# Kernel optimization log

Hardware: AMD Instinct MI355X
Metric: run time of the kernel (lower is better)

## Reference

```python
import jax, jax.numpy as jnp
import numpy as np

B, N, E, H, HEADS = 4, 10000, 160000, 128, 4
NEG_SLOPE = 0.2  # PyG GATConv default
LN_EPS = 1e-5


def setup_inputs() -> dict:
    key = jax.random.key(0)
    ks = jax.random.split(key, 24)
    inp = {}
    inp["node_embeddings"] = jax.random.normal(ks[0], (B, N, H), dtype=jnp.float32)
    inp["src_index"] = jax.random.randint(ks[1], (B, E), 0, N)
    inp["tgt_index"] = jax.random.randint(ks[2], (B, E), 0, N)
    sc = 1.0 / np.sqrt(H)
    for i in range(3):
        j = 3 + 3 * i
        inp[f"W{i+1}"] = jax.random.normal(ks[j], (H, HEADS * H), dtype=jnp.float32) * sc
        inp[f"att_src{i+1}"] = jax.random.normal(ks[j + 1], (HEADS, H), dtype=jnp.float32) * sc
        inp[f"att_dst{i+1}"] = jax.random.normal(ks[j + 2], (HEADS, H), dtype=jnp.float32) * sc
        inp[f"bias{i+1}"] = jnp.zeros((H,), dtype=jnp.float32)
    inp["ln1_g"] = jnp.ones((H,), dtype=jnp.float32)
    inp["ln1_b"] = jnp.zeros((H,), dtype=jnp.float32)
    inp["ln2_g"] = jnp.ones((H,), dtype=jnp.float32)
    inp["ln2_b"] = jnp.zeros((H,), dtype=jnp.float32)
    return inp


def _layer_norm(x, g, b):
    mu = jnp.mean(x, axis=-1, keepdims=True)
    var = jnp.mean((x - mu) ** 2, axis=-1, keepdims=True)
    return (x - mu) * jax.lax.rsqrt(var + LN_EPS) * g + b


def _gat(x, src, tgt, W, a_s, a_d, b):
    # x: [N, H]; src/tgt: [E'] (self-loops already appended). eval mode -> no dropout.
    h = (x @ W).reshape(N, HEADS, H)               # [N, heads, H]
    e_src = jnp.einsum('nhc,hc->nh', h, a_s)       # [N, heads]
    e_dst = jnp.einsum('nhc,hc->nh', h, a_d)
    e = jax.nn.leaky_relu(e_src[src] + e_dst[tgt], NEG_SLOPE)  # [E', heads]
    m = jax.ops.segment_max(e, tgt, num_segments=N)            # per-target max
    ex = jnp.exp(e - m[tgt])
    s = jax.ops.segment_sum(ex, tgt, num_segments=N)
    alpha = ex / s[tgt]                                        # [E', heads]
    out = jax.ops.segment_sum(alpha[:, :, None] * h[src], tgt, num_segments=N)
    return out.mean(axis=1) + b                                # concat=False -> head mean


def reference(node_embeddings, src_index, tgt_index,
              W1, att_src1, att_dst1, bias1,
              W2, att_src2, att_dst2, bias2,
              W3, att_src3, att_dst3, bias3,
              ln1_g, ln1_b, ln2_g, ln2_b):
    loop = jnp.arange(N, dtype=src_index.dtype)

    def one_graph(x, src, tgt):
        s = jnp.concatenate([src, loop])   # GATConv add_self_loops=True (default)
        t = jnp.concatenate([tgt, loop])
        m = _gat(x, s, t, W1, att_src1, att_dst1, bias1)
        m = jax.nn.relu(_layer_norm(m, ln1_g, ln1_b))
        m = _gat(m, s, t, W2, att_src2, att_dst2, bias2)
        m = jax.nn.relu(_layer_norm(m, ln2_g, ln2_b))
        m = _gat(m, s, t, W3, att_src3, att_dst3, bias3)
        return m

    return jax.vmap(one_graph)(node_embeddings, src_index, tgt_index)
```

## Files before the change

### kernel.cpp

```cpp
#include <hip/hip_runtime.h>
#include <hip/hip_bf16.h>
#include <cstdint>
#include <cstddef>

#define B_ 4
#define N_ 10000
#define E_ 160000
#define H_ 128
#define HEADS_ 4
#define HH_ 512
#define NROWS (B_*N_)

typedef __attribute__((ext_vector_type(8))) short bf16x8;
typedef __attribute__((ext_vector_type(4))) float f32x4;
typedef __attribute__((ext_vector_type(2))) float f32x2;

__device__ __forceinline__ float lrelu(float x){ return x > 0.f ? x : 0.2f*x; }
__device__ __forceinline__ unsigned short f2b(float f){
  unsigned int u = __builtin_bit_cast(unsigned int, f);
  unsigned int r = (u + 0x7fffu + ((u >> 16) & 1u)) >> 16;
  return (unsigned short)r;
}
__device__ __forceinline__ float blo(unsigned int u){ return __builtin_bit_cast(float, u << 16); }
__device__ __forceinline__ float bhi(unsigned int u){ return __builtin_bit_cast(float, u & 0xffff0000u); }

__device__ __forceinline__ void acc_row(f32x2* ac, float al, uint4 h){
  f32x2 v = {al, al};
  ac[0] += v * (f32x2){blo(h.x), bhi(h.x)};
  ac[1] += v * (f32x2){blo(h.y), bhi(h.y)};
  ac[2] += v * (f32x2){blo(h.z), bhi(h.z)};
  ac[3] += v * (f32x2){blo(h.w), bhi(h.w)};
}

__global__ void k_count(const int* __restrict__ tgt, int* __restrict__ cnt){
  int e = blockIdx.x*blockDim.x + threadIdx.x;
  int b = blockIdx.y;
  int t = tgt[(size_t)b*E_ + e];
  atomicAdd(&cnt[b*N_ + t], 1);
}

__global__ void k_scan(const int* __restrict__ cnt, int* __restrict__ off, int* __restrict__ cursor){
  int b = blockIdx.x;
  __shared__ int wsum[16];
  __shared__ int carry_s;
  int lane = threadIdx.x & 63, wid = threadIdx.x >> 6;
  if (threadIdx.x == 0){ carry_s = 0; off[b*(N_+1)] = 0; }
  __syncthreads();
  for (int base = 0; base < N_; base += 1024){
    int i = base + threadIdx.x;
    int v = (i < N_) ? cnt[b*N_ + i] : 0;
    int x = v;
    #pragma unroll
    for (int d = 1; d < 64; d <<= 1){
      int y = __shfl_up(x, d);
      if (lane >= d) x += y;
    }
    if (lane == 63) wsum[wid] = x;
    __syncthreads();
    if (wid == 0 && lane < 16){
      int w = wsum[lane];
      #pragma unroll
      for (int d = 1; d < 16; d <<= 1){
        int y = __shfl_up(w, d, 16);
        if (lane >= d) w += y;
      }
      wsum[lane] = w;
    }
    __syncthreads();
    int excl = (wid ? wsum[wid-1] : 0) + carry_s;
    if (i < N_){
      int inc = x + excl;
      off[b*(N_+1) + i + 1] = inc;
      cursor[b*N_ + i] = inc - v;
    }
    __syncthreads();
    if (threadIdx.x == 0) carry_s += wsum[15];
    __syncthreads();
  }
}

__global__ void k_scatter(const int* __restrict__ src, const int* __restrict__ tgt,
                          int* __restrict__ cursor, int* __restrict__ csr){
  int e = blockIdx.x*blockDim.x + threadIdx.x;
  int b = blockIdx.y;
  int t = tgt[(size_t)b*E_ + e];
  int pos = atomicAdd(&cursor[b*N_ + t], 1);
  csr[(size_t)b*E_ + pos] = src[(size_t)b*E_ + e];
}

__global__ void k_prep(const float* __restrict__ W0, const float* __restrict__ W1, const float* __restrict__ W2,
                       const float* __restrict__ as0, const float* __restrict__ as1, const float* __restrict__ as2,
                       const float* __restrict__ ad0, const float* __restrict__ ad1, const float* __restrict__ ad2,
                       float* __restrict__ wasA, float* __restrict__ wadA, unsigned short* __restrict__ wtA){
  int l = blockIdx.y;
  const float* W   = (l==0)?W0:(l==1)?W1:W2;
  const float* asp = (l==0)?as0:(l==1)?as1:as2;
  const float* adp = (l==0)?ad0:(l==1)?ad1:ad2;
  if (blockIdx.x < 256){
    int i = blockIdx.x*256 + threadIdx.x;
    int c = i >> 7, k = i & 127;
    wtA[(size_t)l*HH_*H_ + i] = f2b(W[(size_t)k*HH_ + c]);
  } else {
    int j = (blockIdx.x - 256)*256 + threadIdx.x;
    if (j < H_*HEADS_){
      int k = j >> 2, h = j & 3;
      const float* wrow = W + (size_t)k*HH_ + h*H_;
      const float* asr = asp + h*H_;
      const float* adr = adp + h*H_;
      float ss = 0.f, sd = 0.f;
      for (int c = 0; c < H_; ++c){ float w = wrow[c]; ss += w*asr[c]; sd += w*adr[c]; }
      wasA[l*HH_ + j] = ss; wadA[l*HH_ + j] = sd;
    }
  }
}

__global__ __launch_bounds__(256) void k_cast_logits(const float* __restrict__ X,
    const float* __restrict__ was, const float* __restrict__ wad,
    unsigned short* __restrict__ Xb, float* __restrict__ es, float* __restrict__ ed){
  int gw = (blockIdx.x*blockDim.x + threadIdx.x) >> 6;
  int lane = threadIdx.x & 63;
  float2 v = *(const float2*)(X + (size_t)gw*H_ + lane*2);
  unsigned int o = ((unsigned int)f2b(v.y) << 16) | (unsigned int)f2b(v.x);
  *(unsigned int*)(Xb + (size_t)gw*H_ + lane*2) = o;
  int c = lane*2;
  const f32x4* w4 = (const f32x4*)was;
  const f32x4* d4 = (const f32x4*)wad;
  f32x4 se = v.x*w4[c] + v.y*w4[c+1];
  f32x4 de = v.x*d4[c] + v.y*d4[c+1];
  #pragma unroll
  for (int d = 1; d < 64; d <<= 1){
    se.x += __shfl_xor(se.x,d); se.y += __shfl_xor(se.y,d);
    se.z += __shfl_xor(se.z,d); se.w += __shfl_xor(se.w,d);
    de.x += __shfl_xor(de.x,d); de.y += __shfl_xor(de.y,d);
    de.z += __shfl_xor(de.z,d); de.w += __shfl_xor(de.w,d);
  }
  if (lane == 0){
    *(float4*)(es + (size_t)gw*4) = make_float4(se.x, se.y, se.z, se.w);
    *(float4*)(ed + (size_t)gw*4) = make_float4(de.x, de.y, de.z, de.w);
  }
}

__global__ __launch_bounds__(256) void k_gemm_mfma(const unsigned short* __restrict__ Xb,
    const unsigned short* __restrict__ Wt, unsigned short* __restrict__ Hb){
  __shared__ unsigned short xs[64*128];
  __shared__ unsigned short ws[2][64*128];
  int idx = blockIdx.x;
  int g = (idx & 7) >> 1;
  int j = ((idx >> 3) << 1) | (idx & 1);
  if (j >= 157) return;
  int rmax = N_ - j*64; if (rmax > 64) rmax = 64;
  size_t row0 = (size_t)g*N_ + (size_t)j*64;
  int tid = threadIdx.x;
  int ch = tid & 15, r0 = tid >> 4;
  #pragma unroll
  for (int p = 0; p < 4; ++p){
    int r = r0 + p*16;
    int rr = (r < rmax) ? r : 0;
    int sc = ch ^ (r & 7);
    *(uint4*)(&xs[r*128 + sc*8]) = *(const uint4*)(Xb + (row0 + rr)*H_ + ch*8);
    *(uint4*)(&ws[0][r*128 + sc*8]) = *(const uint4*)(Wt + (size_t)r*H_ + ch*8);
  }
  __syncthreads();
  int w = tid >> 6, l = tid & 63;
  int lr = l & 15, q = l >> 4;
  int arow = w*16 + lr;
  bf16x8 afr[4];
  #pragma unroll
  for (int kf = 0; kf < 4; ++kf){
    int bch = kf*4 + q;
    afr[kf] = *(const bf16x8*)(&xs[arow*128 + (bch ^ (arow & 7))*8]);
  }
  __syncthreads();
  unsigned short* cs = xs;
  #pragma unroll
  for (int cbk = 0; cbk < 8; ++cbk){
    int cur = cbk & 1;
    if (cbk < 7){
      #pragma unroll
      for (int p = 0; p < 4; ++p){
        int r = r0 + p*16;
        int sc = ch ^ (r & 7);
        *(uint4*)(&ws[cur^1][r*128 + sc*8]) =
            *(const uint4*)(Wt + (size_t)((cbk+1)*64 + r)*H_ + ch*8);
      }
    }
    f32x4 z = {0.f, 0.f, 0.f, 0.f};
    f32x4 acc[4] = {z, z, z, z};
    #pragma unroll
    for (int kf = 0; kf < 4; ++kf){
      int bch = kf*4 + q;
      #pragma unroll
      for (int cf = 0; cf < 4; ++cf){
        int brow = cf*16 + lr;
        bf16x8 bfr = *(const bf16x8*)(&ws[cur][brow*128 + (bch ^ (brow & 7))*8]);
        acc[cf] = __builtin_amdgcn_mfma_f32_16x16x32_bf16(afr[kf], bfr, acc[cf], 0, 0, 0);
      }
    }
    #pragma unroll
    for (int cf = 0; cf < 4; ++cf)
      #pragma unroll
      for (int rg = 0; rg < 4; ++rg)
        cs[(w*16 + q*4 + rg)*72 + cf*16 + lr] = f2b(acc[cf][rg]);
    __syncthreads();
    #pragma unroll
    for (int p = 0; p < 2; ++p){
      int k = tid + p*256;
      int r = k >> 3, c8 = k & 7;
      if (r < rmax){
        uint4 v = *(const uint4*)(&cs[r*72 + c8*8]);
        *(uint4*)(Hb + (row0 + r)*HH_ + cbk*64 + c8*8) = v;
      }
    }
    __syncthreads();
  }
}

__global__ __launch_bounds__(256) void k_aggregate(const unsigned short* __restrict__ Hb,
    const float* __restrict__ es, const float* __restrict__ ed,
    const int* __restrict__ off, const int* __restrict__ csr,
    const float* __restrict__ bias, float* __restrict__ Y){
  int idx = blockIdx.x;
  int b = (idx & 7) >> 1;
  int j = ((idx >> 3) << 1) | (idx & 1);
  int lane = threadIdx.x & 63;
  int t = j*4 + (threadIdx.x >> 6);
  int gw = b*N_ + t;
  const float4 edv = *(const float4*)(ed + (size_t)gw*4);
  int start = off[b*(N_+1) + t];
  int deg = off[b*(N_+1) + t + 1] - start;
  const int* lst = csr + (size_t)b*E_ + start;

  float m0=-1e30f, m1=-1e30f, m2=-1e30f, m3=-1e30f;
  float s0=0.f, s1=0.f, s2=0.f, s3=0.f;
  for (int i = lane; i <= deg; i += 64){
    int srcn = (i < deg) ? lst[i] : t;
    float4 ev = *(const float4*)(es + (size_t)(b*N_ + srcn)*4);
    float e0 = lrelu(ev.x + edv.x);
    float e1 = lrelu(ev.y + edv.y);
    float e2 = lrelu(ev.z + edv.z);
    float e3 = lrelu(ev.w + edv.w);
    float nm;
    nm = fmaxf(m0, e0); s0 = s0*__expf(m0-nm) + __expf(e0-nm); m0 = nm;
    nm = fmaxf(m1, e1); s1 = s1*__expf(m1-nm) + __expf(e1-nm); m1 = nm;
    nm = fmaxf(m2, e2); s2 = s2*__expf(m2-nm) + __expf(e2-nm); m2 = nm;
    nm = fmaxf(m3, e3); s3 = s3*__expf(m3-nm) + __expf(e3-nm); m3 = nm;
  }
  #pragma unroll
  for (int d = 1; d < 64; d <<= 1){
    float om, os, nm;
    om = __shfl_xor(m0, d); os = __shfl_xor(s0, d); nm = fmaxf(m0, om);
    s0 = s0*__expf(m0-nm) + os*__expf(om-nm); m0 = nm;
    om = __shfl_xor(m1, d); os = __shfl_xor(s1, d); nm = fmaxf(m1, om);
    s1 = s1*__expf(m1-nm) + os*__expf(om-nm); m1 = nm;
    om = __shfl_xor(m2, d); os = __shfl_xor(s2, d); nm = fmaxf(m2, om);
    s2 = s2*__expf(m2-nm) + os*__expf(om-nm); m2 = nm;
    om = __shfl_xor(m3, d); os = __shfl_xor(s3, d); nm = fmaxf(m3, om);
    s3 = s3*__expf(m3-nm) + os*__expf(om-nm); m3 = nm;
  }

  int head = lane >> 4;
  float mh, sh, edh;
  if      (head == 0){ mh = m0; sh = s0; edh = edv.x; }
  else if (head == 1){ mh = m1; sh = s1; edh = edv.y; }
  else if (head == 2){ mh = m2; sh = s2; edh = edv.z; }
  else               { mh = m3; sh = s3; edh = edv.w; }
  float Lh = mh + __logf(sh);
  int cb = head*H_ + (lane & 15)*8;
  const unsigned short* hbase = Hb + (size_t)b*N_*HH_;
  const float* esb = es + (size_t)b*N_*4;
  f32x2 zz = {0.f, 0.f};
  f32x2 ac[4] = {zz, zz, zz, zz};
  int total = deg + 1;
  int i = 0;
  for (; i + 1 < total; i += 2){
    int sA = lst[i];
    int sB = (i + 1 < deg) ? lst[i+1] : t;
    float eA = esb[(size_t)sA*4 + head];
    float eB = esb[(size_t)sB*4 + head];
    uint4 hA = *(const uint4*)(hbase + (size_t)sA*HH_ + cb);
    uint4 hB = *(const uint4*)(hbase + (size_t)sB*HH_ + cb);
    float aA = __expf(lrelu(eA + edh) - Lh);
    float aB = __expf(lrelu(eB + edh) - Lh);
    acc_row(ac, aA, hA);
    acc_row(ac, aB, hB);
  }
  if (i < total){
    int sA = (i < deg) ? lst[i] : t;
    float eA = esb[(size_t)sA*4 + head];
    uint4 hA = *(const uint4*)(hbase + (size_t)sA*HH_ + cb);
    float aA = __expf(lrelu(eA + edh) - Lh);
    acc_row(ac, aA, hA);
  }
  float a[8] = {ac[0].x, ac[0].y, ac[1].x, ac[1].y, ac[2].x, ac[2].y, ac[3].x, ac[3].y};
  #pragma unroll
  for (int d = 16; d < 64; d <<= 1)
    #pragma unroll
    for (int j2 = 0; j2 < 8; j2++) a[j2] += __shfl_xor(a[j2], d);
  if (lane < 16){
    int c = lane*8;
    float4 o0 = make_float4(0.25f*a[0]+bias[c+0], 0.25f*a[1]+bias[c+1],
                            0.25f*a[2]+bias[c+2], 0.25f*a[3]+bias[c+3]);
    float4 o1 = make_float4(0.25f*a[4]+bias[c+4], 0.25f*a[5]+bias[c+5],
                            0.25f*a[6]+bias[c+6], 0.25f*a[7]+bias[c+7]);
    *(float4*)(Y + (size_t)gw*H_ + c)     = o0;
    *(float4*)(Y + (size_t)gw*H_ + c + 4) = o1;
  }
}

__global__ __launch_bounds__(256) void k_lnrelu_logits(const float* __restrict__ Y,
    const float* __restrict__ g, const float* __restrict__ bb,
    const float* __restrict__ was, const float* __restrict__ wad,
    unsigned short* __restrict__ Xb, float* __restrict__ es, float* __restrict__ ed){
  int gw = (blockIdx.x*blockDim.x + threadIdx.x) >> 6;
  int lane = threadIdx.x & 63;
  float2 v = *(const float2*)(Y + (size_t)gw*H_ + lane*2);
  float sum = v.x + v.y;
  #pragma unroll
  for (int d = 1; d < 64; d <<= 1) sum += __shfl_xor(sum, d);
  float mu = sum * (1.f/H_);
  float dx = v.x - mu, dy = v.y - mu;
  float vs = dx*dx + dy*dy;
  #pragma unroll
  for (int d = 1; d < 64; d <<= 1) vs += __shfl_xor(vs, d);
  float inv = rsqrtf(vs*(1.f/H_) + 1e-5f);
  float2 gv = *(const float2*)(g + lane*2);
  float2 bv = *(const float2*)(bb + lane*2);
  float ox = fmaxf(dx*inv*gv.x + bv.x, 0.f);
  float oy = fmaxf(dy*inv*gv.y + bv.y, 0.f);
  unsigned int o = ((unsigned int)f2b(oy) << 16) | (unsigned int)f2b(ox);
  *(unsigned int*)(Xb + (size_t)gw*H_ + lane*2) = o;
  int c = lane*2;
  const f32x4* w4 = (const f32x4*)was;
  const f32x4* d4 = (const f32x4*)wad;
  f32x4 se = ox*w4[c] + oy*w4[c+1];
  f32x4 de = ox*d4[c] + oy*d4[c+1];
  #pragma unroll
  for (int d = 1; d < 64; d <<= 1){
    se.x += __shfl_xor(se.x,d); se.y += __shfl_xor(se.y,d);
    se.z += __shfl_xor(se.z,d); se.w += __shfl_xor(se.w,d);
    de.x += __shfl_xor(de.x,d); de.y += __shfl_xor(de.y,d);
    de.z += __shfl_xor(de.z,d); de.w += __shfl_xor(de.w,d);
  }
  if (lane == 0){
    *(float4*)(es + (size_t)gw*4) = make_float4(se.x, se.y, se.z, se.w);
    *(float4*)(ed + (size_t)gw*4) = make_float4(de.x, de.y, de.z, de.w);
  }
}

extern "C" void kernel_launch(void* const* d_in, const int* in_sizes, int n_in,
                              void* d_out, int out_size, void* d_ws, size_t ws_size,
                              hipStream_t stream){
  const float* x0   = (const float*)d_in[0];
  const int*   srcI = (const int*)d_in[1];
  const int*   tgtI = (const int*)d_in[2];
  const float* Wl[3]  = {(const float*)d_in[3], (const float*)d_in[7],  (const float*)d_in[11]};
  const float* asl[3] = {(const float*)d_in[4], (const float*)d_in[8],  (const float*)d_in[12]};
  const float* adl[3] = {(const float*)d_in[5], (const float*)d_in[9],  (const float*)d_in[13]};
  const float* bl[3]  = {(const float*)d_in[6], (const float*)d_in[10], (const float*)d_in[14]};
  const float* lng[2] = {(const float*)d_in[15], (const float*)d_in[17]};
  const float* lnb[2] = {(const float*)d_in[16], (const float*)d_in[18]};

  char* p = (char*)d_ws;
  auto carve = [&](size_t bytes) -> void* {
    void* r = (void*)p; p += (bytes + 255) & ~(size_t)255; return r;
  };
  int*   off    = (int*)carve((size_t)B_*(N_+1)*4);
  int*   cnt    = (int*)carve((size_t)B_*N_*4);
  int*   cursor = (int*)carve((size_t)B_*N_*4);
  int*   csr    = (int*)carve((size_t)B_*E_*4);
  float* es     = (float*)carve((size_t)NROWS*4*4);
  float* ed     = (float*)carve((size_t)NROWS*4*4);
  float* wasA   = (float*)carve((size_t)3*HH_*4);
  float* wadA   = (float*)carve((size_t)3*HH_*4);
  unsigned short* wtA  = (unsigned short*)carve((size_t)3*HH_*H_*2);
  unsigned short* hbuf = (unsigned short*)carve((size_t)NROWS*HH_*2);
  unsigned short* xbf  = (unsigned short*)carve((size_t)NROWS*H_*2);
  float* tbuf   = (float*)carve((size_t)NROWS*H_*4);

  hipMemsetAsync(cnt, 0, (size_t)B_*N_*4, stream);
  k_count  <<<dim3(E_/256, B_), 256, 0, stream>>>(tgtI, cnt);
  k_scan   <<<B_, 1024, 0, stream>>>(cnt, off, cursor);
  k_scatter<<<dim3(E_/256, B_), 256, 0, stream>>>(srcI, tgtI, cursor, csr);
  k_prep   <<<dim3(258, 3), 256, 0, stream>>>(Wl[0], Wl[1], Wl[2],
                                              asl[0], asl[1], asl[2],
                                              adl[0], adl[1], adl[2],
                                              wasA, wadA, wtA);
  k_cast_logits<<<NROWS/4, 256, 0, stream>>>(x0, wasA, wadA, xbf, es, ed);

  for (int l = 0; l < 3; ++l){
    k_gemm_mfma<<<632, 256, 0, stream>>>(xbf, wtA + (size_t)l*HH_*H_, hbuf);
    float* yout = (l == 2) ? (float*)d_out : tbuf;
    k_aggregate<<<NROWS/4, 256, 0, stream>>>(hbuf, es, ed, off, csr, bl[l], yout);
    if (l < 2){
      k_lnrelu_logits<<<NROWS/4, 256, 0, stream>>>(tbuf, lng[l], lnb[l],
          wasA + (size_t)(l+1)*HH_, wadA + (size_t)(l+1)*HH_, xbf, es, ed);
    }
  }
}
```

Baseline: 450.4 us.

## Merge setup kernels into fewer launches and split GEMM columns across blocks

The separate count, weight-prep and input-cast steps are merged into one k_setup launch, and the CSR scatter and initial logit computation are merged into one k_misc launch. This cuts launch count and lets independent work overlap. The initial logits are now computed from the bf16-cast input rather than fp32, which slightly changes numerics. The GEMM now splits the 512 output columns into two halves per row tile, doubling the grid for more parallelism at the cost of loading each X tile twice.

```diff
diff --git a/kernel.cpp b/kernel.cpp
--- a/kernel.cpp
+++ b/kernel.cpp
@@ -32,11 +32,48 @@
   ac[3] += v * (f32x2){blo(h.w), bhi(h.w)};
 }
 
-__global__ void k_count(const int* __restrict__ tgt, int* __restrict__ cnt){
-  int e = blockIdx.x*blockDim.x + threadIdx.x;
-  int b = blockIdx.y;
-  int t = tgt[(size_t)b*E_ + e];
-  atomicAdd(&cnt[b*N_ + t], 1);
+__global__ __launch_bounds__(256) void k_setup(
+    const int* __restrict__ tgt, int* __restrict__ cnt,
+    const float* __restrict__ W0, const float* __restrict__ W1, const float* __restrict__ W2,
+    const float* __restrict__ as0, const float* __restrict__ as1, const float* __restrict__ as2,
+    const float* __restrict__ ad0, const float* __restrict__ ad1, const float* __restrict__ ad2,
+    float* __restrict__ wasA, float* __restrict__ wadA, unsigned short* __restrict__ wtA,
+    const float* __restrict__ X, unsigned short* __restrict__ Xb){
+  int blk = blockIdx.x;
+  int tid = threadIdx.x;
+  if (blk < 2500){
+    int b = blk / 625, eb = blk - b*625;
+    int e = eb*256 + tid;
+    int t = tgt[(size_t)b*E_ + e];
+    atomicAdd(&cnt[b*N_ + t], 1);
+  } else if (blk < 3274){
+    int local = blk - 2500;
+    int l = local / 258, px = local - l*258;
+    const float* W   = (l==0)?W0:(l==1)?W1:W2;
+    const float* asp = (l==0)?as0:(l==1)?as1:as2;
+    const float* adp = (l==0)?ad0:(l==1)?ad1:ad2;
+    if (px < 256){
+      int i = px*256 + tid;
+      int c = i >> 7, k = i & 127;
+      wtA[(size_t)l*HH_*H_ + i] = f2b(W[(size_t)k*HH_ + c]);
+    } else {
+      int j = (px - 256)*256 + tid;
+      if (j < H_*HEADS_){
+        int k = j >> 2, h = j & 3;
+        const float* wrow = W + (size_t)k*HH_ + h*H_;
+        const float* asr = asp + h*H_;
+        const float* adr = adp + h*H_;
+        float ss = 0.f, sd = 0.f;
+        for (int c = 0; c < H_; ++c){ float w = wrow[c]; ss += w*asr[c]; sd += w*adr[c]; }
+        wasA[l*HH_ + j] = ss; wadA[l*HH_ + j] = sd;
+      }
+    }
+  } else {
+    int i = (blk - 3274)*256 + tid;
+    float4 v = ((const float4*)X)[i];
+    ushort4 o; o.x = f2b(v.x); o.y = f2b(v.y); o.z = f2b(v.z); o.w = f2b(v.w);
+    ((ushort4*)Xb)[i] = o;
+  }
 }
 
 __global__ void k_scan(const int* __restrict__ cnt, int* __restrict__ off, int* __restrict__ cursor){
@@ -79,64 +116,41 @@
   }
 }
 
-__global__ void k_scatter(const int* __restrict__ src, const int* __restrict__ tgt,
-                          int* __restrict__ cursor, int* __restrict__ csr){
-  int e = blockIdx.x*blockDim.x + threadIdx.x;
-  int b = blockIdx.y;
-  int t = tgt[(size_t)b*E_ + e];
-  int pos = atomicAdd(&cursor[b*N_ + t], 1);
-  csr[(size_t)b*E_ + pos] = src[(size_t)b*E_ + e];
-}
-
-__global__ void k_prep(const float* __restrict__ W0, const float* __restrict__ W1, const float* __restrict__ W2,
-                       const float* __restrict__ as0, const float* __restrict__ as1, const float* __restrict__ as2,
-                       const float* __restrict__ ad0, const float* __restrict__ ad1, const float* __restrict__ ad2,
-                       float* __restrict__ wasA, float* __restrict__ wadA, unsigned short* __restrict__ wtA){
-  int l = blockIdx.y;
-  const float* W   = (l==0)?W0:(l==1)?W1:W2;
-  const float* asp = (l==0)?as0:(l==1)?as1:as2;
-  const float* adp = (l==0)?ad0:(l==1)?ad1:ad2;
-  if (blockIdx.x < 256){
-    int i = blockIdx.x*256 + threadIdx.x;
-    int c = i >> 7, k = i & 127;
-    wtA[(size_t)l*HH_*H_ + i] = f2b(W[(size_t)k*HH_ + c]);
+__global__ __launch_bounds__(256) void k_misc(
+    const int* __restrict__ src, const int* __restrict__ tgt,
+    int* __restrict__ cursor, int* __restrict__ csr,
+    const unsigned short* __restrict__ Xb,
+    const float* __restrict__ was, const float* __restrict__ wad,
+    float* __restrict__ es, float* __restrict__ ed){
+  int blk = blockIdx.x;
+  int tid = threadIdx.x;
+  if (blk < 2500){
+    int b = blk / 625, eb = blk - b*625;
+    int e = eb*256 + tid;
+    int t = tgt[(size_t)b*E_ + e];
+    int pos = atomicAdd(&cursor[b*N_ + t], 1);
+    csr[(size_t)b*E_ + pos] = src[(size_t)b*E_ + e];
   } else {
-    int j = (blockIdx.x - 256)*256 + threadIdx.x;
-    if (j < H_*HEADS_){
-      int k = j >> 2, h = j & 3;
-      const float* wrow = W + (size_t)k*HH_ + h*H_;
-      const float* asr = asp + h*H_;
-      const float* adr = adp + h*H_;
-      float ss = 0.f, sd = 0.f;
-      for (int c = 0; c < H_; ++c){ float w = wrow[c]; ss += w*asr[c]; sd += w*adr[c]; }
-      wasA[l*HH_ + j] = ss; wadA[l*HH_ + j] = sd;
-    }
-  }
-}
-
-__global__ __launch_bounds__(256) void k_cast_logits(const float* __restrict__ X,
-    const float* __restrict__ was, const float* __restrict__ wad,
-    unsigned short* __restrict__ Xb, float* __restrict__ es, float* __restrict__ ed){
-  int gw = (blockIdx.x*blockDim.x + threadIdx.x) >> 6;
-  int lane = threadIdx.x & 63;
-  float2 v = *(const float2*)(X + (size_t)gw*H_ + lane*2);
-  unsigned int o = ((unsigned int)f2b(v.y) << 16) | (unsigned int)f2b(v.x);
-  *(unsigned int*)(Xb + (size_t)gw*H_ + lane*2) = o;
-  int c = lane*2;
-  const f32x4* w4 = (const f32x4*)was;
-  const f32x4* d4 = (const f32x4*)wad;
-  f32x4 se = v.x*w4[c] + v.y*w4[c+1];
-  f32x4 de = v.x*d4[c] + v.y*d4[c+1];
-  #pragma unroll
-  for (int d = 1; d < 64; d <<= 1){
-    se.x += __shfl_xor(se.x,d); se.y += __shfl_xor(se.y,d);
-    se.z += __shfl_xor(se.z,d); se.w += __shfl_xor(se.w,d);
-    de.x += __shfl_xor(de.x,d); de.y += __shfl_xor(de.y,d);
-    de.z += __shfl_xor(de.z,d); de.w += __shfl_xor(de.w,d);
-  }
-  if (lane == 0){
-    *(float4*)(es + (size_t)gw*4) = make_float4(se.x, se.y, se.z, se.w);
-    *(float4*)(ed + (size_t)gw*4) = make_float4(de.x, de.y, de.z, de.w);
+    int gw = ((blk - 2500)*256 + tid) >> 6;
+    int lane = tid & 63;
+    unsigned int u = *(const unsigned int*)(Xb + (size_t)gw*H_ + lane*2);
+    float xlo = blo(u), xhi = bhi(u);
+    int c = lane*2;
+    const f32x4* w4 = (const f32x4*)was;
+    const f32x4* d4 = (const f32x4*)wad;
+    f32x4 se = xlo*w4[c] + xhi*w4[c+1];
+    f32x4 de = xlo*d4[c] + xhi*d4[c+1];
+    #pragma unroll
+    for (int d = 1; d < 64; d <<= 1){
+      se.x += __shfl_xor(se.x,d); se.y += __shfl_xor(se.y,d);
+      se.z += __shfl_xor(se.z,d); se.w += __shfl_xor(se.w,d);
+      de.x += __shfl_xor(de.x,d); de.y += __shfl_xor(de.y,d);
+      de.z += __shfl_xor(de.z,d); de.w += __shfl_xor(de.w,d);
+    }
+    if (lane == 0){
+      *(float4*)(es + (size_t)gw*4) = make_float4(se.x, se.y, se.z, se.w);
+      *(float4*)(ed + (size_t)gw*4) = make_float4(de.x, de.y, de.z, de.w);
+    }
   }
 }
 
@@ -146,10 +160,12 @@
   __shared__ unsigned short ws[2][64*128];
   int idx = blockIdx.x;
   int g = (idx & 7) >> 1;
-  int j = ((idx >> 3) << 1) | (idx & 1);
+  int colhalf = idx & 1;
+  int j = idx >> 3;
   if (j >= 157) return;
   int rmax = N_ - j*64; if (rmax > 64) rmax = 64;
   size_t row0 = (size_t)g*N_ + (size_t)j*64;
+  int col0 = colhalf*256;
   int tid = threadIdx.x;
   int ch = tid & 15, r0 = tid >> 4;
   #pragma unroll
@@ -158,7 +174,7 @@
     int rr = (r < rmax) ? r : 0;
     int sc = ch ^ (r & 7);
     *(uint4*)(&xs[r*128 + sc*8]) = *(const uint4*)(Xb + (row0 + rr)*H_ + ch*8);
-    *(uint4*)(&ws[0][r*128 + sc*8]) = *(const uint4*)(Wt + (size_t)r*H_ + ch*8);
+    *(uint4*)(&ws[0][r*128 + sc*8]) = *(const uint4*)(Wt + (size_t)(col0 + r)*H_ + ch*8);
   }
   __syncthreads();
   int w = tid >> 6, l = tid & 63;
@@ -173,15 +189,15 @@
   __syncthreads();
   unsigned short* cs = xs;
   #pragma unroll
-  for (int cbk = 0; cbk < 8; ++cbk){
+  for (int cbk = 0; cbk < 4; ++cbk){
     int cur = cbk & 1;
-    if (cbk < 7){
+    if (cbk < 3){
       #pragma unroll
       for (int p = 0; p < 4; ++p){
         int r = r0 + p*16;
         int sc = ch ^ (r & 7);
         *(uint4*)(&ws[cur^1][r*128 + sc*8]) =
-            *(const uint4*)(Wt + (size_t)((cbk+1)*64 + r)*H_ + ch*8);
+            *(const uint4*)(Wt + (size_t)(col0 + (cbk+1)*64 + r)*H_ + ch*8);
       }
     }
     f32x4 z = {0.f, 0.f, 0.f, 0.f};
@@ -208,7 +224,7 @@
       int r = k >> 3, c8 = k & 7;
       if (r < rmax){
         uint4 v = *(const uint4*)(&cs[r*72 + c8*8]);
-        *(uint4*)(Hb + (row0 + r)*HH_ + cbk*64 + c8*8) = v;
+        *(uint4*)(Hb + (row0 + r)*HH_ + col0 + cbk*64 + c8*8) = v;
       }
     }
     __syncthreads();
@@ -378,17 +394,16 @@
   float* tbuf   = (float*)carve((size_t)NROWS*H_*4);
 
   hipMemsetAsync(cnt, 0, (size_t)B_*N_*4, stream);
-  k_count  <<<dim3(E_/256, B_), 256, 0, stream>>>(tgtI, cnt);
-  k_scan   <<<B_, 1024, 0, stream>>>(cnt, off, cursor);
-  k_scatter<<<dim3(E_/256, B_), 256, 0, stream>>>(srcI, tgtI, cursor, csr);
-  k_prep   <<<dim3(258, 3), 256, 0, stream>>>(Wl[0], Wl[1], Wl[2],
-                                              asl[0], asl[1], asl[2],
-                                              adl[0], adl[1], adl[2],
-                                              wasA, wadA, wtA);
-  k_cast_logits<<<NROWS/4, 256, 0, stream>>>(x0, wasA, wadA, xbf, es, ed);
+  k_setup<<<8274, 256, 0, stream>>>(tgtI, cnt,
+                                    Wl[0], Wl[1], Wl[2],
+                                    asl[0], asl[1], asl[2],
+                                    adl[0], adl[1], adl[2],
+                                    wasA, wadA, wtA, x0, xbf);
+  k_scan<<<B_, 1024, 0, stream>>>(cnt, off, cursor);
+  k_misc<<<12500, 256, 0, stream>>>(srcI, tgtI, cursor, csr, xbf, wasA, wadA, es, ed);
 
   for (int l = 0; l < 3; ++l){
-    k_gemm_mfma<<<632, 256, 0, stream>>>(xbf, wtA + (size_t)l*HH_*H_, hbuf);
+    k_gemm_mfma<<<1264, 256, 0, stream>>>(xbf, wtA + (size_t)l*HH_*H_, hbuf);
     float* yout = (l == 2) ? (float*)d_out : tbuf;
     k_aggregate<<<NROWS/4, 256, 0, stream>>>(hbuf, es, ed, off, csr, bl[l], yout);
     if (l < 2){
```

New measurement: 442.1 us. About the same (-1.8%).
